# Optimization experiments

Measured on AMD Instinct MI355X. Metric: run time of the kernel, lower is better.

The kernel has to match this reference:

```python
import jax, jax.numpy as jnp
import numpy as np

N = 100000   # nodes
E = 1600000  # edges
D = 128      # input_dim
H = 128      # hidden_dim
CH = 16      # cluster_hidden_dim
P = 10       # processor_nodes


def setup_inputs() -> dict:
    key = jax.random.key(0)
    ks = jax.random.split(key, 22)
    s = 0.05
    return {
        "x": jax.random.normal(ks[0], (N, D), jnp.float32),
        "edges": jax.random.randint(ks[1], (2, E), 0, N, dtype=jnp.int32),
        "edge_attr": jax.random.uniform(ks[2], (E,), jnp.float32),
        "ready": jax.random.randint(ks[3], (N, 1), 0, 2, dtype=jnp.int32),
        "proc_emb": jax.random.normal(ks[4], (P, 3), jnp.float32),
        # GCN layers (PyG GCNConv: lin without bias, explicit bias added after aggregation)
        "gcn_w": jax.random.normal(ks[5], (2, D, H), jnp.float32) * s,
        "gcn_b": jax.random.normal(ks[6], (2, H), jnp.float32) * s,
        # listmlp: Linear(H,H) -> relu, then Linear(H,1)
        "mlp_w1": jax.random.normal(ks[7], (H, H), jnp.float32) * s,
        "mlp_b1": jax.random.normal(ks[8], (H,), jnp.float32) * s,
        "mlp_w2": jax.random.normal(ks[9], (H, 1), jnp.float32) * s,
        "mlp_b2": jax.random.normal(ks[10], (1,), jnp.float32) * s,
        # listmlp_value: Linear(H,1)
        "val_w": jax.random.normal(ks[11], (H, 1), jnp.float32) * s,
        "val_b": jax.random.normal(ks[12], (1,), jnp.float32) * s,
        # cluster_linear: Linear(3*P, CH)
        "cl_w": jax.random.normal(ks[13], (3 * P, CH), jnp.float32) * s,
        "cl_b": jax.random.normal(ks[14], (CH,), jnp.float32) * s,
        # listmlp_pass: Linear(H+CH,H) -> relu, then Linear(H,1)
        "pass_w1": jax.random.normal(ks[15], (H + CH, H), jnp.float32) * s,
        "pass_b1": jax.random.normal(ks[16], (H,), jnp.float32) * s,
        "pass_w2": jax.random.normal(ks[17], (H, 1), jnp.float32) * s,
        "pass_b2": jax.random.normal(ks[18], (1,), jnp.float32) * s,
    }


def _gcn_layer(x, row, col, w_e, W, b):
    # PyG GCNConv with flow='target_to_source': out[row] += norm_e * (x @ W)[col]
    # gcn_norm with idx=row: deg[i] = sum of edge weights with row==i (self-loops included)
    h = x @ W                                              # [N,H]
    deg = jax.ops.segment_sum(w_e, row, num_segments=N)    # [N]
    dis = jnp.where(deg > 0, jax.lax.rsqrt(deg), 0.0)      # deg^-1/2, inf -> 0
    norm = dis[row] * w_e * dis[col]                       # [E+N]
    msg = h[col] * norm[:, None]                           # [E+N,H] gather
    out = jax.ops.segment_sum(msg, row, num_segments=N)    # [N,H] scatter-add
    return out + b


def _forward(x, edges, edge_attr, ready, proc_emb, gcn_w, gcn_b,
             mlp_w1, mlp_b1, mlp_w2, mlp_b2, val_w, val_b, cl_w, cl_b,
             pass_w1, pass_b1, pass_w2, pass_b2):
    # add self-loops with weight 1 (GCNConv default add_self_loops=True)
    loop = jnp.arange(N, dtype=edges.dtype)
    row = jnp.concatenate([edges[0], loop])
    col = jnp.concatenate([edges[1], loop])
    w_e = jnp.concatenate([edge_attr, jnp.ones((N,), edge_attr.dtype)])

    h = x
    for l in range(2):
        h = jax.nn.relu(_gcn_layer(h, row, col, w_e, gcn_w[l], gcn_b[l]))

    mask = ready[:, 0] > 0                                 # [N] bool
    v = jnp.mean(h, axis=0)                                # [H]
    x_pass = jnp.max(jnp.where(mask[:, None], h, -jnp.inf), axis=0)  # masked max, [H]

    fc = proc_emb.reshape(-1) @ cl_w + cl_b                # [CH]
    x_pass = jnp.concatenate([x_pass, fc], axis=0)         # [H+CH]

    v = v @ val_w + val_b                                  # [1]

    logits = jax.nn.relu(h @ mlp_w1 + mlp_b1) @ mlp_w2 + mlp_b2        # [N,1]
    x_pass = jax.nn.relu(x_pass @ pass_w1 + pass_b1) @ pass_w2 + pass_b2  # [1]

    # torch indexes logits[ready]; here we mask non-ready entries with -inf so
    # the softmax over [N+1] matches torch's values on the ready rows.
    node_logits = jnp.where(mask, logits[:, 0], -jnp.inf)
    probs = jax.nn.softmax(jnp.concatenate([node_logits, x_pass], axis=0))  # [N+1]
    return probs, v


def reference(x, edges, edge_attr, ready, proc_emb, gcn_w, gcn_b,
              mlp_w1, mlp_b1, mlp_w2, mlp_b2, val_w, val_b, cl_w, cl_b,
              pass_w1, pass_b1, pass_w2, pass_b2):
    return _forward(x, edges, edge_attr, ready, proc_emb, gcn_w, gcn_b,
                    mlp_w1, mlp_b1, mlp_w2, mlp_b2, val_w, val_b, cl_w, cl_b,
                    pass_w1, pass_b1, pass_w2, pass_b2)
```

## Files before the change

### kernel.cpp

```cpp
#include <hip/hip_runtime.h>
#include <cstdint>

#define NN 100000
#define EE 1600000
#define HH 128
#define NREP 8
#define PSZ (NN / 8)
#define HPP (PSZ / 2)
#define SS 64
#define CAP 300000
#define NBB 500
#define BCH 3200
#define SCAN_CHUNK 512
#define NSCAN ((NN + SCAN_CHUNK - 1) / SCAN_CHUNK)

typedef unsigned long long u64;
typedef unsigned short ushort;
typedef unsigned char uchar;
typedef __attribute__((ext_vector_type(8))) short bf16x8;
typedef __attribute__((ext_vector_type(4))) float f32x4;
typedef __attribute__((ext_vector_type(2))) float f32x2;

__device__ __forceinline__ ushort f2bf(float x) {
    union { float f; unsigned u; } v; v.f = x;
    unsigned r = v.u + 0x7fffu + ((v.u >> 16) & 1u);
    return (ushort)(r >> 16);
}
__device__ __forceinline__ float bf2f(unsigned h16) {
    union { unsigned u; float f; } v; v.u = h16 << 16; return v.f;
}

__device__ __forceinline__ uchar f2fp8(float a) {
    return (uchar)(__builtin_amdgcn_cvt_pk_fp8_f32(a, a, 0, false) & 0xff);
}
__device__ __forceinline__ void unpack8_fp8(uint2 q, float* v) {
    f32x2 a = __builtin_amdgcn_cvt_pk_f32_fp8(q.x, false);
    f32x2 b = __builtin_amdgcn_cvt_pk_f32_fp8(q.x, true);
    f32x2 c = __builtin_amdgcn_cvt_pk_f32_fp8(q.y, false);
    f32x2 d = __builtin_amdgcn_cvt_pk_f32_fp8(q.y, true);
    v[0] = a[0]; v[1] = a[1]; v[2] = b[0]; v[3] = b[1];
    v[4] = c[0]; v[5] = c[1]; v[6] = d[0]; v[7] = d[1];
}

__device__ __forceinline__ unsigned encf(float f) {
    int b = __float_as_int(f);
    return (b >= 0) ? ((unsigned)b | 0x80000000u) : ~(unsigned)b;
}
__device__ __forceinline__ float decf(unsigned u) {
    return (u & 0x80000000u) ? __int_as_float((int)(u & 0x7fffffffu))
                             : __int_as_float((int)(~u));
}
#define ENC_NEG_INF 0x007FFFFFu

__global__ void k_setup(float* __restrict__ meansum, unsigned* __restrict__ maxenc,
                        unsigned* __restrict__ lmaxenc, float* __restrict__ esum,
                        int* __restrict__ gtail,
                        const float* __restrict__ w0, const float* __restrict__ w1,
                        const float* __restrict__ w2, ushort* __restrict__ wt) {
    int idx = blockIdx.x * blockDim.x + threadIdx.x;
    if (idx < NREP * HH) { meansum[idx] = 0.f; maxenc[idx] = ENC_NEG_INF; }
    if (idx < 8) gtail[idx] = 0;
    if (idx == 0) { lmaxenc[0] = ENC_NEG_INF; esum[0] = 0.f; }
    if (idx < 3 * HH * HH) {
        int mat = idx >> 14;
        int e = idx & 16383;
        int n = e >> 7, k = e & 127;
        const float* src = (mat == 0) ? w0 : (mat == 1) ? w1 : w2;
        wt[idx] = f2bf(src[k * HH + n]);
    }
}

__global__ __launch_bounds__(256) void k_bucket(const int* __restrict__ rows,
                                                const int* __restrict__ cols,
                                                const float* __restrict__ ea,
                                                int* __restrict__ gtail,
                                                u64* __restrict__ ebuck) {
    __shared__ u64 buf[8][1024];
    __shared__ int cnt8[8];
    __shared__ int rsv[8];
    int t = threadIdx.x;
    if (t < 8) cnt8[t] = 0;
    __syncthreads();
    int e0 = blockIdx.x * BCH;
    int e1 = e0 + BCH;
    for (int ebase = e0; ebase < e1; ebase += 1024) {
        int e = ebase + t * 4;
        if (e < e1) {
            int4 r4 = *(const int4*)(rows + e);
            int4 c4 = *(const int4*)(cols + e);
            float4 a4 = *(const float4*)(ea + e);
            int rr[4] = {r4.x, r4.y, r4.z, r4.w};
            int cc[4] = {c4.x, c4.y, c4.z, c4.w};
            float aa[4] = {a4.x, a4.y, a4.z, a4.w};
#pragma unroll
            for (int j = 0; j < 4; ++j) {
                int p = rr[j] / PSZ;
                int rl = rr[j] - p * PSZ;
                unsigned q = (unsigned)(aa[j] * 32767.0f + 0.5f);
                u64 en = ((u64)rl << 32) | (u64)(((unsigned)cc[j] << 15) | q);
                int idx = atomicAdd(&cnt8[p], 1);
                buf[p][idx] = en;
            }
        }
        __syncthreads();
        if (t < 8) rsv[t] = atomicAdd(&gtail[t], cnt8[t]);
        __syncthreads();
#pragma unroll
        for (int p = 0; p < 8; ++p) {
            int nn = cnt8[p], oo = rsv[p];
            u64* dst = ebuck + (size_t)p * CAP + oo;
            for (int j = t; j < nn; j += 256) dst[j] = buf[p][j];
        }
        __syncthreads();
        if (t < 8) cnt8[t] = 0;
        __syncthreads();
    }
}

__global__ __launch_bounds__(256) void k_cnt2(const u64* __restrict__ ebuck,
                                              const int* __restrict__ gtail,
                                              unsigned* __restrict__ cntp) {
    __shared__ unsigned h32[HPP];
    int b = blockIdx.x;
    int s = b >> 3, p = b & 7;
    for (int j = threadIdx.x; j < HPP; j += 256) h32[j] = 0;
    __syncthreads();
    int pc = gtail[p];
    int len = (pc + SS - 1) / SS;
    int lo = s * len, hi = min(lo + len, pc);
    const u64* src = ebuck + (size_t)p * CAP;
    for (int i = lo + threadIdx.x; i < hi; i += 256) {
        int rl = (int)(src[i] >> 32);
        atomicAdd(&h32[rl >> 1], (rl & 1) ? 0x10000u : 1u);
    }
    __syncthreads();
    unsigned* dst = cntp + (size_t)(p * SS + s) * HPP;
    for (int j = threadIdx.x; j < HPP; j += 256) dst[j] = h32[j];
}

__global__ void k_rowdelta(const unsigned* __restrict__ cntp, int* __restrict__ count,
                           unsigned* __restrict__ deltap) {
    int rp = blockIdx.x * blockDim.x + threadIdx.x;
    if (rp >= NN / 2) return;
    int p = rp / HPP, j = rp - p * HPP;
    unsigned s0 = 0, s1 = 0;
#pragma unroll 8
    for (int c = 0; c < SS; ++c) {
        size_t o = (size_t)(p * SS + c) * HPP + j;
        unsigned v = cntp[o];
        deltap[o] = s0 | (s1 << 16);
        s0 += v & 0xffffu;
        s1 += v >> 16;
    }
    int r0 = p * PSZ + 2 * j;
    *(int2*)(count + r0) = make_int2((int)s0, (int)s1);
}

__global__ void k_scan1(const int* __restrict__ cnt, int* __restrict__ out,
                        int* __restrict__ bsum) {
    int b = blockIdx.x, t = threadIdx.x;
    int i0 = b * SCAN_CHUNK + t * 2;
    int c0 = (i0 < NN) ? cnt[i0] : 0;
    int c1 = (i0 + 1 < NN) ? cnt[i0 + 1] : 0;
    int s = c0 + c1;
    int lane = t & 63, w = t >> 6;
    int v = s;
#pragma unroll
    for (int off = 1; off < 64; off <<= 1) {
        int u = __shfl_up(v, off, 64);
        if (lane >= off) v += u;
    }
    __shared__ int wsum[4];
    if (lane == 63) wsum[w] = v;
    __syncthreads();
    int wadd = 0;
    for (int j = 0; j < w; ++j) wadd += wsum[j];
    int incl = v + wadd;
    int excl = incl - s;
    if (i0 < NN) out[i0] = excl;
    if (i0 + 1 < NN) out[i0 + 1] = excl + c0;
    if (t == 255) bsum[b] = incl;
}

__global__ void k_scan2(int* __restrict__ bsum) {
    __shared__ int tmp[256];
    int t = threadIdx.x;
    int v = (t < NSCAN) ? bsum[t] : 0;
    tmp[t] = v;
    __syncthreads();
    for (int off = 1; off < 256; off <<= 1) {
        int u = (t >= off) ? tmp[t - off] : 0;
        __syncthreads();
        tmp[t] += u;
        __syncthreads();
    }
    if (t < NSCAN) bsum[t] = tmp[t] - v;
}

__global__ void k_scan3(int* __restrict__ out, const int* __restrict__ bsum) {
    int i = blockIdx.x * blockDim.x + threadIdx.x;
    if (i < NN) out[i] += bsum[i / SCAN_CHUNK];
    if (i == 0) out[NN] = EE;
}

__global__ __launch_bounds__(256) void k_fill2(const u64* __restrict__ ebuck,
                                               const int* __restrict__ gtail,
                                               const unsigned* __restrict__ deltap,
                                               const int* __restrict__ base,
                                               unsigned* __restrict__ csre) {
    __shared__ int nxt[PSZ];
    int b = blockIdx.x;
    int s = b >> 3, p = b & 7;
    const unsigned* dsrc = deltap + (size_t)(p * SS + s) * HPP;
    const int* bsrc = base + p * PSZ;
    for (int j = threadIdx.x; j < HPP; j += 256) {
        unsigned d = dsrc[j];
        int2 bb = *(const int2*)(bsrc + 2 * j);
        nxt[2 * j] = bb.x + (int)(d & 0xffffu);
        nxt[2 * j + 1] = bb.y + (int)(d >> 16);
    }
    __syncthreads();
    int pc = gtail[p];
    int len = (pc + SS - 1) / SS;
    int lo = s * len, hi = min(lo + len, pc);
    const u64* src = ebuck + (size_t)p * CAP;
    for (int i = lo + threadIdx.x; i < hi; i += 256) {
        u64 en = src[i];
        int rl = (int)(en >> 32);
        int slot = atomicAdd(&nxt[rl], 1);
        csre[slot] = (unsigned)(en & 0xffffffffu);
    }
}

__global__ void k_degsum(const unsigned* __restrict__ csre, const int* __restrict__ base,
                         float* __restrict__ dis) {
    int r = blockIdx.x * blockDim.x + threadIdx.x;
    if (r >= NN) return;
    int lo = base[r], hi = base[r + 1];
    float s = 0.f;
    for (int e = lo; e < hi; ++e) s += (float)(csre[e] & 0x7fffu);
    dis[r] = rsqrtf(1.0f + s * (1.0f / 32767.0f));
}

__global__ __launch_bounds__(256) void k_gather(const uchar* __restrict__ hW,
                                                const unsigned* __restrict__ csre,
                                                const int* __restrict__ base,
                                                const float* __restrict__ dis,
                                                const float* __restrict__ bias,
                                                ushort* __restrict__ agg) {
    int node = blockIdx.x * 16 + (threadIdx.x >> 4);
    if (node >= NN) return;
    int l = threadIdx.x & 15;
    int f = l * 8;
    int lo = base[node], hi = base[node + 1];
    float disn = dis[node];
    float wk = disn * (1.0f / 32767.0f);
    float acc[8];
    {
        uint2 q = *(const uint2*)(hW + (size_t)node * HH + f);
        float v[8]; unpack8_fp8(q, v);
#pragma unroll
        for (int j = 0; j < 8; ++j) acc[j] = disn * v[j];
    }
    for (int eb = lo; eb < hi; eb += 8) {
        unsigned pp[8];
#pragma unroll
        for (int j = 0; j < 8; ++j)
            pp[j] = csre[min(eb + j, hi - 1)];
        uint2 qq[8];
#pragma unroll
        for (int j = 0; j < 8; ++j)
            qq[j] = *(const uint2*)(hW + (size_t)(pp[j] >> 15) * HH + f);
#pragma unroll
        for (int j = 0; j < 8; ++j) {
            float w = (eb + j < hi) ? (float)(pp[j] & 0x7fffu) * wk : 0.f;
            float v[8]; unpack8_fp8(qq[j], v);
#pragma unroll
            for (int k = 0; k < 8; ++k) acc[k] += w * v[k];
        }
    }
    float4 b0 = *(const float4*)(bias + f);
    float4 b1 = *(const float4*)(bias + f + 4);
    ushort o[8];
    o[0] = f2bf(acc[0] + b0.x); o[1] = f2bf(acc[1] + b0.y);
    o[2] = f2bf(acc[2] + b0.z); o[3] = f2bf(acc[3] + b0.w);
    o[4] = f2bf(acc[4] + b1.x); o[5] = f2bf(acc[5] + b1.y);
    o[6] = f2bf(acc[6] + b1.z); o[7] = f2bf(acc[7] + b1.w);
    *(uint4*)(agg + (size_t)node * HH + f) = *(uint4*)o;
}

template <int MODE>
__global__ __launch_bounds__(256) void k_mfma(const void* __restrict__ Ain,
                                              const ushort* __restrict__ Wt,
                                              uchar* __restrict__ C,
                                              const float* __restrict__ dis,
                                              const float* __restrict__ b1,
                                              const float* __restrict__ w2v,
                                              const float* __restrict__ b2,
                                              const int* __restrict__ ready,
                                              float* __restrict__ logits,
                                              float* __restrict__ meansum,
                                              unsigned* __restrict__ maxenc,
                                              unsigned* __restrict__ lmaxenc, int n) {
    __shared__ ushort As[64 * HH];
    __shared__ ushort Ws[128 * HH];
    __shared__ int rdy[64];
    __shared__ unsigned slmax;
    const int t = threadIdx.x;
    const int rb = blockIdx.x * 64;
    if (MODE == 2) {
        if (t < 64) rdy[t] = (rb + t < n) ? ready[rb + t] : 0;
        if (t == 0) slmax = ENC_NEG_INF;
    }
#pragma unroll
    for (int i = 0; i < 8; ++i) {
        int nr = i * 16 + (t >> 4);
        int gc = t & 15;
        uint4 q = *(const uint4*)(Wt + (size_t)nr * HH + gc * 8);
        *(uint4*)(Ws + nr * HH + ((gc ^ (nr & 15)) * 8)) = q;
    }
#pragma unroll
    for (int i = 0; i < 4; ++i) {
        int m = i * 16 + (t >> 4);
        int k = (t & 15) * 8;
        ushort pk[8];
        if (MODE == 0) {
            const float* Af = (const float*)Ain;
            float4 v0 = make_float4(0.f, 0.f, 0.f, 0.f), v1 = v0;
            if (rb + m < n) {
                const float* src = Af + (size_t)(rb + m) * HH + k;
                v0 = *(const float4*)src;
                v1 = *(const float4*)(src + 4);
            }
            pk[0] = f2bf(v0.x); pk[1] = f2bf(v0.y); pk[2] = f2bf(v0.z); pk[3] = f2bf(v0.w);
            pk[4] = f2bf(v1.x); pk[5] = f2bf(v1.y); pk[6] = f2bf(v1.z); pk[7] = f2bf(v1.w);
        } else {
            const ushort* Au = (const ushort*)Ain;
            uint4 q = make_uint4(0, 0, 0, 0);
            if (rb + m < n) q = *(const uint4*)(Au + (size_t)(rb + m) * HH + k);
            *(uint4*)pk = q;
#pragma unroll
            for (int j = 0; j < 8; ++j) pk[j] = (pk[j] & 0x8000) ? (ushort)0 : pk[j];
        }
        int gsw = (t & 15) ^ (m & 15);
        *(uint4*)(As + m * HH + gsw * 8) = *(uint4*)pk;
    }
    __syncthreads();

    const int wave = t >> 6, lane = t & 63;
    const int cl = lane & 15;
    const int kq = lane >> 4;
    const int m0 = wave * 16;

    f32x4 acc[8];
#pragma unroll
    for (int c = 0; c < 8; ++c) acc[c] = (f32x4){0.f, 0.f, 0.f, 0.f};

    const int am = m0 + cl;
#pragma unroll
    for (int kk = 0; kk < 4; ++kk) {
        int g = kk * 4 + kq;
        bf16x8 a = *(const bf16x8*)(As + am * HH + ((g ^ cl) * 8));
#pragma unroll
        for (int c = 0; c < 8; ++c) {
            bf16x8 b = *(const bf16x8*)(Ws + (c * 16 + cl) * HH + ((g ^ cl) * 8));
            acc[c] = __builtin_amdgcn_mfma_f32_16x16x32_bf16(a, b, acc[c], 0, 0, 0);
        }
    }

    if (MODE < 2) {
#pragma unroll
        for (int r = 0; r < 4; ++r) {
            int row = rb + m0 + kq * 4 + r;
            if (row < n) {
                float dsc = dis[row];
#pragma unroll
                for (int c = 0; c < 8; ++c)
                    C[(size_t)row * HH + c * 16 + cl] = f2fp8(acc[c][r] * dsc);
            }
        }
    } else {
        float b1c[8], w2c[8];
#pragma unroll
        for (int c = 0; c < 8; ++c) { b1c[c] = b1[c * 16 + cl]; w2c[c] = w2v[c * 16 + cl]; }
        const float b2s = b2[0];
        unsigned mylmax = ENC_NEG_INF;
#pragma unroll
        for (int r = 0; r < 4; ++r) {
            float s = 0.f;
#pragma unroll
            for (int c = 0; c < 8; ++c)
                s += fmaxf(acc[c][r] + b1c[c], 0.f) * w2c[c];
            s += __shfl_xor(s, 1, 64);
            s += __shfl_xor(s, 2, 64);
            s += __shfl_xor(s, 4, 64);
            s += __shfl_xor(s, 8, 64);
            if (cl == 0) {
                int rloc = m0 + kq * 4 + r;
                int row = rb + rloc;
                if (row < n) {
                    float lg = s + b2s;
                    logits[row] = lg;
                    if (rdy[rloc] > 0) {
                        unsigned e = encf(lg);
                        if (e > mylmax) mylmax = e;
                    }
                }
            }
        }
        if (cl == 0 && mylmax != ENC_NEG_INF) atomicMax(&slmax, mylmax);

        int lim = min(64, n - rb);
        if (t < HH) {
            int f = t, gf = f >> 3, fo = f & 7;
            float sum = 0.f, mx = -3.4e38f;
            for (int m = 0; m < lim; ++m) {
                float v = bf2f(As[m * HH + ((gf ^ (m & 15)) * 8) + fo]);
                sum += v;
                if (rdy[m] > 0) mx = fmaxf(mx, v);
            }
            int rep = blockIdx.x & (NREP - 1);
            atomicAdd(&meansum[rep * HH + f], sum);
            if (mx > -3.0e38f) atomicMax(&maxenc[rep * HH + f], encf(mx));
        }
        __syncthreads();
        if (t == 0 && slmax != ENC_NEG_INF) atomicMax(lmaxenc, slmax);
    }
}

__global__ void k_fin1(const float* __restrict__ meansum, const unsigned* __restrict__ maxenc,
                       const unsigned* __restrict__ lmaxenc,
                       const float* __restrict__ val_w, const float* __restrict__ val_b,
                       const float* __restrict__ pe, const float* __restrict__ cl_w,
                       const float* __restrict__ cl_b, const float* __restrict__ pw1,
                       const float* __restrict__ pb1, const float* __restrict__ pw2,
                       const float* __restrict__ pb2, float* __restrict__ scal,
                       float* __restrict__ d_out) {
    __shared__ float xp[144];
    __shared__ float msum[HH];
    __shared__ float zp[HH];
    int t = threadIdx.x;
    if (t < HH) {
        float s = 0.f;
        unsigned mx = ENC_NEG_INF;
#pragma unroll
        for (int r = 0; r < NREP; ++r) {
            s += meansum[r * HH + t];
            unsigned e = maxenc[r * HH + t];
            if (e > mx) mx = e;
        }
        msum[t] = s;
        xp[t] = decf(mx);
    } else if (t < 144) {
        int c = t - HH;
        float s = cl_b[c];
        for (int k = 0; k < 30; ++k) s += pe[k] * cl_w[k * 16 + c];
        xp[t] = s;
    }
    __syncthreads();
    if (t < HH) {
        float s = pb1[t];
        for (int k = 0; k < 144; ++k) s += xp[k] * pw1[k * HH + t];
        zp[t] = fmaxf(s, 0.f);
    }
    __syncthreads();
    if (t < 64) {
        float s1 = zp[t] * pw2[t] + zp[t + 64] * pw2[t + 64];
        float s2 = msum[t] * val_w[t] + msum[t + 64] * val_w[t + 64];
#pragma unroll
        for (int off = 32; off > 0; off >>= 1) {
            s1 += __shfl_xor(s1, off, 64);
            s2 += __shfl_xor(s2, off, 64);
        }
        if (t == 0) {
            float xpass = s1 + pb2[0];
            float v = s2 * (1.0f / NN) + val_b[0];
            float M = fmaxf(decf(lmaxenc[0]), xpass);
            scal[0] = M;
            scal[1] = expf(xpass - M);
            d_out[NN + 1] = v;
        }
    }
}

__global__ __launch_bounds__(256) void k_exp(const float* __restrict__ logits,
                                             const int* __restrict__ ready,
                                             const float* __restrict__ scal,
                                             float* __restrict__ d_out,
                                             float* __restrict__ esum) {
    __shared__ float warr[4];
    int t = threadIdx.x;
    int i = blockIdx.x * 256 + t;
    float M = scal[0];
    float p = 0.f;
    if (i < NN) {
        if (ready[i] > 0) p = expf(logits[i] - M);
        d_out[i] = p;
    }
    float s = p;
#pragma unroll
    for (int off = 32; off > 0; off >>= 1) s += __shfl_xor(s, off, 64);
    if ((t & 63) == 0) warr[t >> 6] = s;
    __syncthreads();
    if (t == 0) atomicAdd(esum, warr[0] + warr[1] + warr[2] + warr[3]);
}

__global__ void k_scale(const float* __restrict__ esum, const float* __restrict__ scal,
                        float* __restrict__ d_out) {
    int i = blockIdx.x * blockDim.x + threadIdx.x;
    float inv = 1.0f / (esum[0] + scal[1]);
    if (i < NN) d_out[i] *= inv;
    else if (i == NN) d_out[NN] = scal[1] * inv;
}

extern "C" void kernel_launch(void* const* d_in, const int* in_sizes, int n_in,
                              void* d_out, int out_size, void* d_ws, size_t ws_size,
                              hipStream_t stream) {
    const float* x      = (const float*)d_in[0];
    const int*   edges  = (const int*)d_in[1];
    const float* eattr  = (const float*)d_in[2];
    const int*   ready  = (const int*)d_in[3];
    const float* pe     = (const float*)d_in[4];
    const float* gcn_w  = (const float*)d_in[5];
    const float* gcn_b  = (const float*)d_in[6];
    const float* mlp_w1 = (const float*)d_in[7];
    const float* mlp_b1 = (const float*)d_in[8];
    const float* mlp_w2 = (const float*)d_in[9];
    const float* mlp_b2 = (const float*)d_in[10];
    const float* val_w  = (const float*)d_in[11];
    const float* val_b  = (const float*)d_in[12];
    const float* cl_w   = (const float*)d_in[13];
    const float* cl_b   = (const float*)d_in[14];
    const float* pw1    = (const float*)d_in[15];
    const float* pb1    = (const float*)d_in[16];
    const float* pw2    = (const float*)d_in[17];
    const float* pb2    = (const float*)d_in[18];

    const int* rows = edges;
    const int* cols = edges + EE;

    char* P = (char*)d_ws;
    size_t off = 0;
    auto carve = [&](size_t bytes) {
        off = (off + 255) & ~(size_t)255;
        void* p = P + off;
        off += bytes;
        return p;
    };
    float* dis     = (float*)carve(NN * 4);
    float* logits  = (float*)carve(NN * 4);
    int*   count   = (int*)carve(NN * 4);
    int*   base    = (int*)carve((NN + 1) * 4);
    int*   bsum    = (int*)carve(256 * 4);
    ushort* bufB   = (ushort*)carve((size_t)NN * HH * 2);
    uchar* bufH    = (uchar*)carve((size_t)NN * HH);
    unsigned* csre = (unsigned*)carve((size_t)EE * 4);
    u64*   ebuck   = (u64*)carve((size_t)8 * CAP * 8);
    float* meansum = (float*)carve(NREP * HH * 4);
    unsigned* maxenc = (unsigned*)carve(NREP * HH * 4);
    unsigned* lmaxenc = (unsigned*)carve(4);
    float* esum    = (float*)carve(4);
    float* scal    = (float*)carve(8);
    int*   gtail   = (int*)carve(8 * 4);
    ushort* wt     = (ushort*)carve(3 * HH * HH * 2);

    unsigned* cntp   = (unsigned*)bufB;
    unsigned* deltap = (unsigned*)bufB + (size_t)8 * SS * HPP;

    float* out = (float*)d_out;

    const int nb = (NN + 255) / 256;
    const int gb = (NN + 63) / 64;
    const int ab = (NN + 15) / 16;
    const int pb = 8 * SS;

    k_setup<<<(3 * HH * HH + 255) / 256, 256, 0, stream>>>(meansum, maxenc, lmaxenc, esum,
                                                           gtail, gcn_w, gcn_w + HH * HH,
                                                           mlp_w1, wt);

    k_bucket<<<NBB, 256, 0, stream>>>(rows, cols, eattr, gtail, ebuck);
    k_cnt2<<<pb, 256, 0, stream>>>(ebuck, gtail, cntp);
    k_rowdelta<<<(NN / 2 + 255) / 256, 256, 0, stream>>>(cntp, count, deltap);
    k_scan1<<<NSCAN, 256, 0, stream>>>(count, base, bsum);
    k_scan2<<<1, 256, 0, stream>>>(bsum);
    k_scan3<<<nb, 256, 0, stream>>>(base, bsum);
    k_fill2<<<pb, 256, 0, stream>>>(ebuck, gtail, deltap, base, csre);
    k_degsum<<<nb, 256, 0, stream>>>(csre, base, dis);

    k_mfma<0><<<gb, 256, 0, stream>>>(x, wt, bufH, dis, nullptr, nullptr, nullptr, nullptr,
                                      nullptr, nullptr, nullptr, nullptr, NN);
    k_gather<<<ab, 256, 0, stream>>>(bufH, csre, base, dis, gcn_b, bufB);

    k_mfma<1><<<gb, 256, 0, stream>>>(bufB, wt + HH * HH, bufH, dis, nullptr, nullptr, nullptr,
                                      nullptr, nullptr, nullptr, nullptr, nullptr, NN);
    k_gather<<<ab, 256, 0, stream>>>(bufH, csre, base, dis, gcn_b + HH, bufB);

    k_mfma<2><<<gb, 256, 0, stream>>>(bufB, wt + 2 * HH * HH, nullptr, nullptr, mlp_b1, mlp_w2,
                                      mlp_b2, ready, logits, meansum, maxenc, lmaxenc, NN);
    k_fin1<<<1, 256, 0, stream>>>(meansum, maxenc, lmaxenc, val_w, val_b, pe, cl_w, cl_b,
                                  pw1, pb1, pw2, pb2, scal, out);
    k_exp<<<nb, 256, 0, stream>>>(logits, ready, scal, out, esum);
    k_scale<<<(NN + 1 + 255) / 256, 256, 0, stream>>>(esum, scal, out);
}
```

Baseline: 337.6 us.

## Pad CSR rows to multiples of 8, warp-aggregate bucket atomics, transpose MFMA epilogue

Each CSR row segment is padded to a multiple of 8 entries. The padding slots are filled with zero-weight self references so the gather kernel can load edge words with two uint4 loads and drop its bounds masks. The bucket kernel replaces per-element shared atomics with ballot-based warp aggregation per partition. The MFMA kernel swaps operand order so each lane owns one node row, which allows packed fp8 stores and a cheaper logits reduction. These changes add padded memory traffic and extra ballot loops per element.

```diff
diff --git a/kernel.cpp b/kernel.cpp
--- a/kernel.cpp
+++ b/kernel.cpp
@@ -79,27 +79,43 @@
     __shared__ int cnt8[8];
     __shared__ int rsv[8];
     int t = threadIdx.x;
+    int lane = t & 63;
+    u64 mask_lt = (lane == 0) ? 0ull : ((1ull << lane) - 1ull);
     if (t < 8) cnt8[t] = 0;
     __syncthreads();
     int e0 = blockIdx.x * BCH;
     int e1 = e0 + BCH;
     for (int ebase = e0; ebase < e1; ebase += 1024) {
         int e = ebase + t * 4;
-        if (e < e1) {
+        bool act = e < e1;
+        int rr[4] = {0, 0, 0, 0};
+        int cc[4] = {0, 0, 0, 0};
+        float aa[4] = {0.f, 0.f, 0.f, 0.f};
+        if (act) {
             int4 r4 = *(const int4*)(rows + e);
             int4 c4 = *(const int4*)(cols + e);
             float4 a4 = *(const float4*)(ea + e);
-            int rr[4] = {r4.x, r4.y, r4.z, r4.w};
-            int cc[4] = {c4.x, c4.y, c4.z, c4.w};
-            float aa[4] = {a4.x, a4.y, a4.z, a4.w};
-#pragma unroll
-            for (int j = 0; j < 4; ++j) {
-                int p = rr[j] / PSZ;
-                int rl = rr[j] - p * PSZ;
-                unsigned q = (unsigned)(aa[j] * 32767.0f + 0.5f);
-                u64 en = ((u64)rl << 32) | (u64)(((unsigned)cc[j] << 15) | q);
-                int idx = atomicAdd(&cnt8[p], 1);
-                buf[p][idx] = en;
+            rr[0] = r4.x; rr[1] = r4.y; rr[2] = r4.z; rr[3] = r4.w;
+            cc[0] = c4.x; cc[1] = c4.y; cc[2] = c4.z; cc[3] = c4.w;
+            aa[0] = a4.x; aa[1] = a4.y; aa[2] = a4.z; aa[3] = a4.w;
+        }
+#pragma unroll
+        for (int j = 0; j < 4; ++j) {
+            int p = act ? (rr[j] / PSZ) : -1;
+            int rl = rr[j] - ((p < 0) ? 0 : p) * PSZ;
+            unsigned q = (unsigned)(aa[j] * 32767.0f + 0.5f);
+            u64 en = ((u64)rl << 32) | (u64)(((unsigned)cc[j] << 15) | q);
+#pragma unroll
+            for (int pp = 0; pp < 8; ++pp) {
+                u64 m = __ballot(p == pp);
+                if (m) {
+                    int leader = __ffsll((long long)m) - 1;
+                    int cnt = __popcll(m);
+                    int bi = 0;
+                    if (lane == leader) bi = atomicAdd(&cnt8[pp], cnt);
+                    bi = __shfl(bi, leader, 64);
+                    if (p == pp) buf[pp][bi + __popcll(m & mask_lt)] = en;
+                }
             }
         }
         __syncthreads();
@@ -162,6 +178,8 @@
     int i0 = b * SCAN_CHUNK + t * 2;
     int c0 = (i0 < NN) ? cnt[i0] : 0;
     int c1 = (i0 + 1 < NN) ? cnt[i0 + 1] : 0;
+    c0 = (c0 + 7) & ~7;
+    c1 = (c1 + 7) & ~7;
     int s = c0 + c1;
     int lane = t & 63, w = t >> 6;
     int v = s;
@@ -182,7 +200,7 @@
     if (t == 255) bsum[b] = incl;
 }
 
-__global__ void k_scan2(int* __restrict__ bsum) {
+__global__ void k_scan2(int* __restrict__ bsum, int* __restrict__ base) {
     __shared__ int tmp[256];
     int t = threadIdx.x;
     int v = (t < NSCAN) ? bsum[t] : 0;
@@ -194,13 +212,13 @@
         tmp[t] += u;
         __syncthreads();
     }
+    if (t == NSCAN - 1) base[NN] = tmp[t];
     if (t < NSCAN) bsum[t] = tmp[t] - v;
 }
 
 __global__ void k_scan3(int* __restrict__ out, const int* __restrict__ bsum) {
     int i = blockIdx.x * blockDim.x + threadIdx.x;
     if (i < NN) out[i] += bsum[i / SCAN_CHUNK];
-    if (i == 0) out[NN] = EE;
 }
 
 __global__ __launch_bounds__(256) void k_fill2(const u64* __restrict__ ebuck,
@@ -232,13 +250,16 @@
     }
 }
 
-__global__ void k_degsum(const unsigned* __restrict__ csre, const int* __restrict__ base,
-                         float* __restrict__ dis) {
+__global__ void k_degsum(const int* __restrict__ count, unsigned* __restrict__ csre,
+                         const int* __restrict__ base, float* __restrict__ dis) {
     int r = blockIdx.x * blockDim.x + threadIdx.x;
     if (r >= NN) return;
-    int lo = base[r], hi = base[r + 1];
+    int lo = base[r], hip = base[r + 1];
+    int hireal = lo + count[r];
     float s = 0.f;
-    for (int e = lo; e < hi; ++e) s += (float)(csre[e] & 0x7fffu);
+    for (int e = lo; e < hireal; ++e) s += (float)(csre[e] & 0x7fffu);
+    unsigned selfv = (unsigned)r << 15;
+    for (int e = hireal; e < hip; ++e) csre[e] = selfv;
     dis[r] = rsqrtf(1.0f + s * (1.0f / 32767.0f));
 }
 
@@ -263,17 +284,16 @@
         for (int j = 0; j < 8; ++j) acc[j] = disn * v[j];
     }
     for (int eb = lo; eb < hi; eb += 8) {
-        unsigned pp[8];
-#pragma unroll
-        for (int j = 0; j < 8; ++j)
-            pp[j] = csre[min(eb + j, hi - 1)];
+        uint4 pa = *(const uint4*)(csre + eb);
+        uint4 pb = *(const uint4*)(csre + eb + 4);
+        unsigned pp[8] = {pa.x, pa.y, pa.z, pa.w, pb.x, pb.y, pb.z, pb.w};
         uint2 qq[8];
 #pragma unroll
         for (int j = 0; j < 8; ++j)
             qq[j] = *(const uint2*)(hW + (size_t)(pp[j] >> 15) * HH + f);
 #pragma unroll
         for (int j = 0; j < 8; ++j) {
-            float w = (eb + j < hi) ? (float)(pp[j] & 0x7fffu) * wk : 0.f;
+            float w = (float)(pp[j] & 0x7fffu) * wk;
             float v[8]; unpack8_fp8(qq[j], v);
 #pragma unroll
             for (int k = 0; k < 8; ++k) acc[k] += w * v[k];
@@ -356,59 +376,49 @@
 #pragma unroll
     for (int c = 0; c < 8; ++c) acc[c] = (f32x4){0.f, 0.f, 0.f, 0.f};
 
-    const int am = m0 + cl;
 #pragma unroll
     for (int kk = 0; kk < 4; ++kk) {
         int g = kk * 4 + kq;
-        bf16x8 a = *(const bf16x8*)(As + am * HH + ((g ^ cl) * 8));
+        bf16x8 bfr = *(const bf16x8*)(As + (m0 + cl) * HH + ((g ^ cl) * 8));
 #pragma unroll
         for (int c = 0; c < 8; ++c) {
-            bf16x8 b = *(const bf16x8*)(Ws + (c * 16 + cl) * HH + ((g ^ cl) * 8));
-            acc[c] = __builtin_amdgcn_mfma_f32_16x16x32_bf16(a, b, acc[c], 0, 0, 0);
-        }
-    }
-
+            bf16x8 afr = *(const bf16x8*)(Ws + (c * 16 + cl) * HH + ((g ^ cl) * 8));
+            acc[c] = __builtin_amdgcn_mfma_f32_16x16x32_bf16(afr, bfr, acc[c], 0, 0, 0);
+        }
+    }
+
+    const int node = rb + m0 + cl;
     if (MODE < 2) {
-#pragma unroll
-        for (int r = 0; r < 4; ++r) {
-            int row = rb + m0 + kq * 4 + r;
-            if (row < n) {
-                float dsc = dis[row];
-#pragma unroll
-                for (int c = 0; c < 8; ++c)
-                    C[(size_t)row * HH + c * 16 + cl] = f2fp8(acc[c][r] * dsc);
+        if (node < n) {
+            float d = dis[node];
+            uchar* dst = C + (size_t)node * HH + kq * 4;
+#pragma unroll
+            for (int c = 0; c < 8; ++c) {
+                unsigned u = __builtin_amdgcn_cvt_pk_fp8_f32(acc[c][0] * d, acc[c][1] * d, 0u, false);
+                u = __builtin_amdgcn_cvt_pk_fp8_f32(acc[c][2] * d, acc[c][3] * d, u, true);
+                *(unsigned*)(dst + c * 16) = u;
             }
         }
     } else {
-        float b1c[8], w2c[8];
-#pragma unroll
-        for (int c = 0; c < 8; ++c) { b1c[c] = b1[c * 16 + cl]; w2c[c] = w2v[c * 16 + cl]; }
-        const float b2s = b2[0];
+        float s = 0.f;
+#pragma unroll
+        for (int c = 0; c < 8; ++c) {
+            float4 bb = *(const float4*)(b1 + c * 16 + kq * 4);
+            float4 ww = *(const float4*)(w2v + c * 16 + kq * 4);
+            s += fmaxf(acc[c][0] + bb.x, 0.f) * ww.x;
+            s += fmaxf(acc[c][1] + bb.y, 0.f) * ww.y;
+            s += fmaxf(acc[c][2] + bb.z, 0.f) * ww.z;
+            s += fmaxf(acc[c][3] + bb.w, 0.f) * ww.w;
+        }
+        s += __shfl_xor(s, 16, 64);
+        s += __shfl_xor(s, 32, 64);
         unsigned mylmax = ENC_NEG_INF;
-#pragma unroll
-        for (int r = 0; r < 4; ++r) {
-            float s = 0.f;
-#pragma unroll
-            for (int c = 0; c < 8; ++c)
-                s += fmaxf(acc[c][r] + b1c[c], 0.f) * w2c[c];
-            s += __shfl_xor(s, 1, 64);
-            s += __shfl_xor(s, 2, 64);
-            s += __shfl_xor(s, 4, 64);
-            s += __shfl_xor(s, 8, 64);
-            if (cl == 0) {
-                int rloc = m0 + kq * 4 + r;
-                int row = rb + rloc;
-                if (row < n) {
-                    float lg = s + b2s;
-                    logits[row] = lg;
-                    if (rdy[rloc] > 0) {
-                        unsigned e = encf(lg);
-                        if (e > mylmax) mylmax = e;
-                    }
-                }
-            }
-        }
-        if (cl == 0 && mylmax != ENC_NEG_INF) atomicMax(&slmax, mylmax);
+        if (kq == 0 && node < n) {
+            float lg = s + b2[0];
+            logits[node] = lg;
+            if (rdy[m0 + cl] > 0) mylmax = encf(lg);
+        }
+        if (mylmax != ENC_NEG_INF) atomicMax(&slmax, mylmax);
 
         int lim = min(64, n - rb);
         if (t < HH) {
@@ -554,7 +564,7 @@
     int*   bsum    = (int*)carve(256 * 4);
     ushort* bufB   = (ushort*)carve((size_t)NN * HH * 2);
     uchar* bufH    = (uchar*)carve((size_t)NN * HH);
-    unsigned* csre = (unsigned*)carve((size_t)EE * 4);
+    unsigned* csre = (unsigned*)carve((size_t)(EE + 8 * NN) * 4);
     u64*   ebuck   = (u64*)carve((size_t)8 * CAP * 8);
     float* meansum = (float*)carve(NREP * HH * 4);
     unsigned* maxenc = (unsigned*)carve(NREP * HH * 4);
@@ -582,10 +592,10 @@
     k_cnt2<<<pb, 256, 0, stream>>>(ebuck, gtail, cntp);
     k_rowdelta<<<(NN / 2 + 255) / 256, 256, 0, stream>>>(cntp, count, deltap);
     k_scan1<<<NSCAN, 256, 0, stream>>>(count, base, bsum);
-    k_scan2<<<1, 256, 0, stream>>>(bsum);
+    k_scan2<<<1, 256, 0, stream>>>(bsum, base);
     k_scan3<<<nb, 256, 0, stream>>>(base, bsum);
     k_fill2<<<pb, 256, 0, stream>>>(ebuck, gtail, deltap, base, csre);
-    k_degsum<<<nb, 256, 0, stream>>>(csre, base, dis);
+    k_degsum<<<nb, 256, 0, stream>>>(count, csre, base, dis);
 
     k_mfma<0><<<gb, 256, 0, stream>>>(x, wt, bufH, dis, nullptr, nullptr, nullptr, nullptr,
                                       nullptr, nullptr, nullptr, nullptr, NN);
```

Result: slower. 351.8 us (+4.2%).
